# Performance work log

Measured on AMD Instinct MI355X. Metric: run time of the kernel, lower is better.

## Reference

```python
import jax, jax.numpy as jnp
import numpy as np

D = 1024       # latent_size
LW = 16        # leaf_width
DEPTH = 8      # tree depth
NN = 2**DEPTH - 1   # internal decision nodes
NL = 2**DEPTH       # leaves
B, S = 2, 1024


def _fff(x, nw, nb, w1, b1, w2, b2, act):
    """Hard-routed Fast FeedForward (eval mode).
    x: (B,S,D); nw: (NN,D); nb: (NN,); w1: (NL,D,LW); b1: (NL,LW);
    w2: (NL,LW,D); b2: (NL,D).
    """
    node = jnp.zeros(x.shape[:2], dtype=jnp.int32)
    for _ in range(DEPTH):
        logit = jnp.einsum('bsd,bsd->bs', x, nw[node]) + nb[node]
        node = 2 * node + 1 + (logit > 0).astype(jnp.int32)
    leaf = node - NN  # (B,S) in [0, NL)
    h = act(jnp.einsum('bsd,bsdl->bsl', x, w1[leaf]) + b1[leaf])
    return jnp.einsum('bsl,bsld->bsd', h, w2[leaf]) + b2[leaf]


def _forward(x,
             q_nw, q_nb, q_w1, q_b1, q_w2, q_b2,
             k_nw, k_nb, k_w1, k_b1, k_w2, k_b2,
             v_nw, v_nb, v_w1, v_b1, v_w2, v_b2,
             f_nw, f_nb, f_w1, f_b1, f_w2, f_b2):
    # manual norm (torch std is unbiased; note original divides by sqrt(std+eps))
    mu = jnp.mean(x, -1, keepdims=True)
    sd = jnp.std(x, -1, ddof=1, keepdims=True)
    xn = (x - mu) / jnp.sqrt(sd + 1e-5)
    relu = jax.nn.relu
    q = _fff(xn, q_nw, q_nb, q_w1, q_b1, q_w2, q_b2, relu)
    k = _fff(xn, k_nw, k_nb, k_w1, k_b1, k_w2, k_b2, relu)
    v = _fff(xn, v_nw, v_nb, v_w1, v_b1, v_w2, v_b2, relu)
    att = jax.nn.softmax(jnp.einsum('bqd,bkd->bqk', q, k) / jnp.sqrt(jnp.float32(D)), axis=-1)
    y = xn + jnp.einsum('bqk,bkd->bqd', att, v)
    gelu = lambda t: jax.nn.gelu(t, approximate=False)
    return y + _fff(y, f_nw, f_nb, f_w1, f_b1, f_w2, f_b2, gelu)


def _make_fff_params(key, scale_in, scale_leaf):
    ks = jax.random.split(key, 4)
    nw = jax.random.normal(ks[0], (NN, D), jnp.float32) * scale_in
    nb = jnp.zeros((NN,), jnp.float32)
    w1 = jax.random.normal(ks[1], (NL, D, LW), jnp.float32) * scale_in
    b1 = jax.random.normal(ks[2], (NL, LW), jnp.float32) * 0.01
    w2 = jax.random.normal(ks[3], (NL, LW, D), jnp.float32) * scale_leaf
    b2 = jnp.zeros((NL, D), jnp.float32)
    return nw, nb, w1, b1, w2, b2


def setup_inputs() -> dict:
    key = jax.random.key(0)
    kx, kq, kk, kv, kf = jax.random.split(key, 5)
    s_in = 1.0 / np.sqrt(D)
    s_lf = 1.0 / np.sqrt(LW)
    inp = {"x": jax.random.normal(kx, (B, S, D), jnp.float32)}
    for name, kk_ in (("q", kq), ("k", kk), ("v", kv), ("f", kf)):
        nw, nb, w1, b1, w2, b2 = _make_fff_params(kk_, s_in, s_lf)
        inp.update({f"{name}_nw": nw, f"{name}_nb": nb, f"{name}_w1": w1,
                    f"{name}_b1": b1, f"{name}_w2": w2, f"{name}_b2": b2})
    return inp


def reference(x,
              q_nw, q_nb, q_w1, q_b1, q_w2, q_b2,
              k_nw, k_nb, k_w1, k_b1, k_w2, k_b2,
              v_nw, v_nb, v_w1, v_b1, v_w2, v_b2,
              f_nw, f_nb, f_w1, f_b1, f_w2, f_b2):
    return _forward(x,
                    q_nw, q_nb, q_w1, q_b1, q_w2, q_b2,
                    k_nw, k_nb, k_w1, k_b1, k_w2, k_b2,
                    v_nw, v_nb, v_w1, v_b1, v_w2, v_b2,
                    f_nw, f_nb, f_w1, f_b1, f_w2, f_b2)
```

## Files before the change

kernel.cpp:

```cpp
#include <hip/hip_runtime.h>
#include <hip/hip_bf16.h>
#include <math.h>

#define DD 1024
#define LWW 16
#define NNODES 255
#define NLEAF 256
#define BB 2
#define SS 1024
#define NTOK (BB*SS)
#define PLANE ((size_t)NTOK * DD)
#define MS ((size_t)1024 * 1024)
#define MAXCHUNK 512
#define CH 8

typedef short bf16x8 __attribute__((ext_vector_type(8)));
typedef float f32x4 __attribute__((ext_vector_type(4)));

#define GLOBAL_AS __attribute__((address_space(1)))
#define LDS_AS __attribute__((address_space(3)))

__device__ __forceinline__ void gld_lds16(const void* g, void* l) {
  __builtin_amdgcn_global_load_lds((const GLOBAL_AS unsigned int*)g,
                                   (LDS_AS unsigned int*)l, 16, 0, 0);
}

__device__ __forceinline__ unsigned short f2bf(float f) {
  union { float f; unsigned int u; } v; v.f = f;
  unsigned int u = v.u;
  unsigned int lsb = (u >> 16) & 1u;
  u += 0x7fffu + lsb;
  return (unsigned short)(u >> 16);
}
__device__ __forceinline__ float bf2f(unsigned short h) {
  union { unsigned int u; float f; } v; v.u = ((unsigned int)h) << 16;
  return v.f;
}
__device__ __forceinline__ void split3(float a, unsigned short& h0,
                                       unsigned short& h1, unsigned short& h2) {
  h0 = f2bf(a);
  float r = a - bf2f(h0);
  h1 = f2bf(r);
  float r2 = r - bf2f(h1);
  h2 = f2bf(r2);
}

__global__ __launch_bounds__(256) void norm_kernel(const float* __restrict__ x,
                                                   float* __restrict__ xn) {
  int tok = blockIdx.x, tid = threadIdx.x;
  const float4 v = ((const float4*)(x + (size_t)tok * DD))[tid];
  double s = (double)v.x + (double)v.y + (double)v.z + (double)v.w;
  double s2 = (double)v.x * v.x + (double)v.y * v.y + (double)v.z * v.z + (double)v.w * v.w;
  for (int o = 32; o; o >>= 1) { s += __shfl_down(s, o); s2 += __shfl_down(s2, o); }
  __shared__ double rs[4], rs2[4];
  __shared__ float stats[2];
  int wid = tid >> 6, lane = tid & 63;
  if (lane == 0) { rs[wid] = s; rs2[wid] = s2; }
  __syncthreads();
  if (tid == 0) {
    double ts = rs[0] + rs[1] + rs[2] + rs[3];
    double ts2 = rs2[0] + rs2[1] + rs2[2] + rs2[3];
    double mu = ts / DD;
    double var = (ts2 - DD * mu * mu) / (DD - 1);
    if (var < 0) var = 0;
    double sd = sqrt(var);
    stats[0] = (float)mu;
    stats[1] = (float)(1.0 / sqrt(sd + 1e-5));
  }
  __syncthreads();
  float mu = stats[0], inv = stats[1];
  float4 o;
  o.x = (v.x - mu) * inv; o.y = (v.y - mu) * inv;
  o.z = (v.z - mu) * inv; o.w = (v.w - mu) * inv;
  ((float4*)(xn + (size_t)tok * DD))[tid] = o;
}

__global__ __launch_bounds__(256) void route_kernel(
    const float* __restrict__ xin,
    const float* nw0, const float* nb0,
    const float* nw1, const float* nb1,
    const float* nw2, const float* nb2,
    int* __restrict__ leaf_arr, int* __restrict__ hist, int ntree) {
  int tid = threadIdx.x, lane = tid & 63, wid = tid >> 6;
  int gw = blockIdx.x * 4 + wid;
  int tok = gw / ntree, tr = gw - tok * ntree;
  if (tok >= NTOK) return;
  const float* nws[3] = {nw0, nw1, nw2};
  const float* nbs[3] = {nb0, nb1, nb2};
  const float* nw = nws[tr];
  const float* nb = nbs[tr];
  f32x4 xq[4];
  const f32x4* xb = (const f32x4*)(xin + (size_t)tok * DD);
#pragma unroll
  for (int j = 0; j < 4; ++j) xq[j] = xb[lane + 64 * j];
  int node = 0;
#pragma unroll 1
  for (int step = 0; step < 8; ++step) {
    const f32x4* wb = (const f32x4*)(nw + (size_t)node * DD);
    double p = 0.0;
#pragma unroll
    for (int j = 0; j < 4; ++j) {
      f32x4 w = wb[lane + 64 * j];
      p += (double)xq[j][0] * w[0] + (double)xq[j][1] * w[1] +
           (double)xq[j][2] * w[2] + (double)xq[j][3] * w[3];
    }
#pragma unroll
    for (int o = 1; o < 64; o <<= 1) p += __shfl_xor(p, o);
    double logit = p + (double)nb[node];
    node = 2 * node + 1 + (logit > 0.0 ? 1 : 0);
  }
  if (lane == 0) {
    int leaf = node - NNODES;
    leaf_arr[(size_t)tr * NTOK + tok] = leaf;
    atomicAdd(&hist[tr * NLEAF + leaf], 1);
  }
}

__global__ __launch_bounds__(256) void scan_kernel(const int* __restrict__ hist,
                                                   int* __restrict__ offs,
                                                   int* __restrict__ cursor,
                                                   int4* __restrict__ desc,
                                                   int ntree, int tree0) {
  __shared__ int buf[256];
  __shared__ int dcnt;
  int tid = threadIdx.x;
  for (int tr = 0; tr < ntree; ++tr) {
    int slot = tree0 + tr;
    int v = hist[slot * NLEAF + tid];
    buf[tid] = v;
    if (tid == 0) dcnt = 0;
    __syncthreads();
    int run = v;
    for (int off = 1; off < 256; off <<= 1) {
      int add = (tid >= off) ? buf[tid - off] : 0;
      __syncthreads();
      run += add;
      buf[tid] = run;
      __syncthreads();
    }
    if (tid == 0) offs[slot * (NLEAF + 1)] = 0;
    offs[slot * (NLEAF + 1) + tid + 1] = run;
    cursor[slot * NLEAF + tid] = run - v;
    if (v > 0) {
      int k = (v + CH - 1) / CH;
      int base = atomicAdd(&dcnt, k);
      int lo = run - v;
      for (int j = 0; j < k; ++j) {
        int s = lo + j * CH;
        int e = min(run, s + CH);
        desc[slot * MAXCHUNK + base + j] = make_int4(tid, s, e, 0);
      }
    }
    __syncthreads();
  }
}

__global__ __launch_bounds__(256) void scatter_kernel(const int* __restrict__ leaf_arr,
                                                      int* __restrict__ cursor,
                                                      int* __restrict__ list,
                                                      int tree0, int ntree) {
  int tok = blockIdx.x * 256 + threadIdx.x;
  for (int tr = 0; tr < ntree; ++tr) {
    int slot = tree0 + tr;
    int leaf = leaf_arr[(size_t)slot * NTOK + tok];
    int pos = atomicAdd(&cursor[slot * NLEAF + leaf], 1);
    list[(size_t)slot * NTOK + pos] = tok;
  }
}

struct LeafW {
  const float* w1[3]; const float* b1[3]; const float* w2[3]; const float* b2[3];
  unsigned short* outs[3];
  float* out_res;
};

__global__ __launch_bounds__(256) void leafmlp_kernel(
    const float* __restrict__ xin,
    const int* __restrict__ list, const int4* __restrict__ desc,
    LeafW W, int tree0, int act) {
  int ty = blockIdx.y;
  int slot = tree0 + ty;
  int4 dsc = desc[slot * MAXCHUNK + blockIdx.x];
  int leaf = dsc.x;
  if (leaf < 0) return;
  int lo = dsc.y, hi = dsc.z;
  const int* L = list + (size_t)slot * NTOK;
  const float* W1 = W.w1[ty] + (size_t)leaf * DD * LWW;
  const float* B1 = W.b1[ty] + (size_t)leaf * LWW;
  const float* W2 = W.w2[ty] + (size_t)leaf * LWW * DD;
  const float* B2 = W.b2[ty] + (size_t)leaf * DD;
  unsigned short* osp = W.outs[ty];
  int tid = threadIdx.x;
  int lane = tid & 63, wid = tid >> 6;

  __shared__ float xsl[CH][1024];
  __shared__ float hpart[4][CH][20];
  __shared__ float hs[CH][16];

  float b1c = B1[tid & 15];

  int r = tid >> 2;
  const float* W1p = W1 + (size_t)r * 16 + (tid & 3) * 4;
  f32x4 wreg[16];
#pragma unroll
  for (int p = 0; p < 16; ++p) wreg[p] = *(const f32x4*)(W1p + (size_t)p * 1024);

  int toks[CH];
#pragma unroll
  for (int t = 0; t < CH; ++t) {
    int idx = lo + t;
    toks[t] = (idx < hi) ? L[idx] : -1;
    if (toks[t] >= 0) {
      float4 v = ((const float4*)(xin + (size_t)toks[t] * DD))[tid];
      *(float4*)&xsl[t][tid * 4] = v;
    } else {
      float4 z = {0.f, 0.f, 0.f, 0.f};
      *(float4*)&xsl[t][tid * 4] = z;
    }
  }
  __syncthreads();

  f32x4 part4[CH];
#pragma unroll
  for (int t = 0; t < CH; ++t) part4[t] = (f32x4){0.f, 0.f, 0.f, 0.f};
#pragma unroll
  for (int p = 0; p < 16; ++p) {
#pragma unroll
    for (int t = 0; t < CH; ++t) {
      float xv = xsl[t][p * 64 + r];
      part4[t] += xv * wreg[p];
    }
  }

  const float* W2p = W2 + tid * 4;
  f32x4 w2a[8];
#pragma unroll
  for (int l = 0; l < 8; ++l) w2a[l] = *(const f32x4*)(W2p + (size_t)l * 1024);
  f32x4 b2v = *(const f32x4*)(B2 + tid * 4);

#pragma unroll
  for (int t = 0; t < CH; ++t) {
    f32x4 v = part4[t];
#pragma unroll
    for (int o = 4; o < 64; o <<= 1) {
      v[0] += __shfl_xor(v[0], o);
      v[1] += __shfl_xor(v[1], o);
      v[2] += __shfl_xor(v[2], o);
      v[3] += __shfl_xor(v[3], o);
    }
    if (lane < 4) *(f32x4*)&hpart[wid][t][lane * 4] = v;
  }
  __syncthreads();

  if (tid < 16 * CH) {
    int t = tid >> 4, c = tid & 15;
    float h = b1c + hpart[0][t][c] + hpart[1][t][c] + hpart[2][t][c] + hpart[3][t][c];
    if (act == 0) h = fmaxf(h, 0.f);
    else h = 0.5f * h * (1.f + erff(h * 0.70710678118654752f));
    hs[t][c] = h;
  }
  __syncthreads();

  f32x4 w2b[8];
#pragma unroll
  for (int l = 0; l < 8; ++l) w2b[l] = *(const f32x4*)(W2p + (size_t)(8 + l) * 1024);
  f32x4 acc[CH];
#pragma unroll
  for (int t = 0; t < CH; ++t) acc[t] = b2v;
#pragma unroll
  for (int l = 0; l < 8; ++l) {
#pragma unroll
    for (int t = 0; t < CH; ++t) acc[t] += w2a[l] * hs[t][l];
  }
#pragma unroll
  for (int l = 0; l < 8; ++l) {
#pragma unroll
    for (int t = 0; t < CH; ++t) acc[t] += w2b[l] * hs[t][8 + l];
  }

#pragma unroll
  for (int t = 0; t < CH; ++t) {
    if (toks[t] < 0) break;
    size_t off = (size_t)toks[t] * DD + tid * 4;
    if (osp) {
      ushort4 o0, o1, o2;
      split3(acc[t][0], o0.x, o1.x, o2.x);
      split3(acc[t][1], o0.y, o1.y, o2.y);
      split3(acc[t][2], o0.z, o1.z, o2.z);
      split3(acc[t][3], o0.w, o1.w, o2.w);
      *(ushort4*)(osp + off) = o0;
      *(ushort4*)(osp + PLANE + off) = o1;
      *(ushort4*)(osp + 2 * PLANE + off) = o2;
    } else {
      float4 xr = *(const float4*)&xsl[t][tid * 4];
      float4 o;
      o.x = xr.x + acc[t][0];
      o.y = xr.y + acc[t][1];
      o.z = xr.z + acc[t][2];
      o.w = xr.w + acc[t][3];
      *(float4*)(W.out_res + off) = o;
    }
  }
}

__global__ __launch_bounds__(256) void transpose_v(const unsigned short* __restrict__ v,
                                                   unsigned short* __restrict__ vt) {
  __shared__ unsigned short t[32][34];
  int b = blockIdx.z & 1, p = blockIdx.z >> 1;
  int s0 = blockIdx.x * 32, d0 = blockIdx.y * 32;
  int tx = threadIdx.x, ty = threadIdx.y;
  const unsigned short* vb = v + p * PLANE + (size_t)b * SS * DD;
  unsigned short* vtb = vt + p * PLANE + (size_t)b * DD * SS;
#pragma unroll
  for (int k = 0; k < 4; ++k) {
    int r = ty + 8 * k;
    t[r][tx] = vb[(size_t)(s0 + r) * DD + d0 + tx];
  }
  __syncthreads();
#pragma unroll
  for (int k = 0; k < 4; ++k) {
    int r = ty + 8 * k;
    vtb[(size_t)(d0 + r) * SS + s0 + tx] = t[tx][r];
  }
}

#define BKK 64
__global__ __launch_bounds__(256) void gemm_nt3(
    const unsigned short* __restrict__ A,
    const unsigned short* __restrict__ Bt,
    float* __restrict__ C,
    const float* __restrict__ addsrc,
    float scale) {
  __shared__ short As[3][64 * BKK];
  __shared__ short Bs[3][64 * BKK];
  int b = blockIdx.z;
  int m0 = blockIdx.x * 64, n0 = blockIdx.y * 64;
  int tid = threadIdx.x, lane = tid & 63, wid = tid >> 6;
  int wm = wid >> 1, wn = wid & 1;
  f32x4 acc[2][2] = {};

  int sk0 = (((lane & 7) ^ (lane >> 3)) * 8);
  int srow0 = wid * 8 + (lane >> 3);
  int fr = lane & 15;
  int r7 = fr & 7;

  const unsigned short* Ap[3];
  const unsigned short* Bp[3];
#pragma unroll
  for (int p = 0; p < 3; ++p) {
    Ap[p] = A + p * PLANE + b * MS;
    Bp[p] = Bt + p * PLANE + b * MS;
  }

  for (int kt = 0; kt < 1024 / BKK; ++kt) {
    int kbase = kt * BKK;
#pragma unroll
    for (int p = 0; p < 3; ++p) {
#pragma unroll
      for (int r = 0; r < 2; ++r) {
        int row = r * 32 + srow0;
        gld_lds16(Ap[p] + (size_t)(m0 + row) * 1024 + kbase + sk0, &As[p][(r * 32 + wid * 8) * BKK]);
        gld_lds16(Bp[p] + (size_t)(n0 + row) * 1024 + kbase + sk0, &Bs[p][(r * 32 + wid * 8) * BKK]);
      }
    }
    __syncthreads();
#pragma unroll
    for (int kk = 0; kk < 2; ++kk) {
      int fkc = (((kk * 4 + (lane >> 4)) ^ r7) * 8);
      bf16x8 af[3][2], bfr[3][2];
#pragma unroll
      for (int p = 0; p < 3; ++p) {
        af[p][0]  = *(const bf16x8*)&As[p][(wm * 32 + fr) * BKK + fkc];
        af[p][1]  = *(const bf16x8*)&As[p][(wm * 32 + 16 + fr) * BKK + fkc];
        bfr[p][0] = *(const bf16x8*)&Bs[p][(wn * 32 + fr) * BKK + fkc];
        bfr[p][1] = *(const bf16x8*)&Bs[p][(wn * 32 + 16 + fr) * BKK + fkc];
      }
#pragma unroll
      for (int mi = 0; mi < 2; ++mi)
#pragma unroll
        for (int ni = 0; ni < 2; ++ni) {
          acc[mi][ni] = __builtin_amdgcn_mfma_f32_16x16x32_bf16(af[2][mi], bfr[0][ni], acc[mi][ni], 0, 0, 0);
          acc[mi][ni] = __builtin_amdgcn_mfma_f32_16x16x32_bf16(af[1][mi], bfr[1][ni], acc[mi][ni], 0, 0, 0);
          acc[mi][ni] = __builtin_amdgcn_mfma_f32_16x16x32_bf16(af[0][mi], bfr[2][ni], acc[mi][ni], 0, 0, 0);
          acc[mi][ni] = __builtin_amdgcn_mfma_f32_16x16x32_bf16(af[1][mi], bfr[0][ni], acc[mi][ni], 0, 0, 0);
          acc[mi][ni] = __builtin_amdgcn_mfma_f32_16x16x32_bf16(af[0][mi], bfr[1][ni], acc[mi][ni], 0, 0, 0);
          acc[mi][ni] = __builtin_amdgcn_mfma_f32_16x16x32_bf16(af[0][mi], bfr[0][ni], acc[mi][ni], 0, 0, 0);
        }
    }
    __syncthreads();
  }

  float* Cb = C + b * MS;
  const float* Rb = addsrc ? addsrc + b * MS : nullptr;
  int crow0 = (lane >> 4) * 4, ccol = lane & 15;
#pragma unroll
  for (int mi = 0; mi < 2; ++mi)
#pragma unroll
    for (int ni = 0; ni < 2; ++ni) {
      int colg = n0 + wn * 32 + ni * 16 + ccol;
#pragma unroll
      for (int j = 0; j < 4; ++j) {
        int rowg = m0 + wm * 32 + mi * 16 + crow0 + j;
        float vv = acc[mi][ni][j] * scale;
        if (Rb) vv += Rb[(size_t)rowg * 1024 + colg];
        Cb[(size_t)rowg * 1024 + colg] = vv;
      }
    }
}

__global__ __launch_bounds__(256) void softmax_kernel(const float* __restrict__ sc,
                                                      unsigned short* __restrict__ P) {
  int row = blockIdx.x, tid = threadIdx.x;
  int wid = tid >> 6, lane = tid & 63;
  const float4 v = ((const float4*)(sc + (size_t)row * SS))[tid];
  float mx = fmaxf(fmaxf(v.x, v.y), fmaxf(v.z, v.w));
  for (int o = 32; o; o >>= 1) mx = fmaxf(mx, __shfl_down(mx, o));
  __shared__ float red[4];
  __shared__ float bres[2];
  if (lane == 0) red[wid] = mx;
  __syncthreads();
  if (tid == 0) bres[0] = fmaxf(fmaxf(red[0], red[1]), fmaxf(red[2], red[3]));
  __syncthreads();
  float m = bres[0];
  float e0 = expf(v.x - m), e1 = expf(v.y - m), e2 = expf(v.z - m), e3 = expf(v.w - m);
  float s = e0 + e1 + e2 + e3;
  for (int o = 32; o; o >>= 1) s += __shfl_down(s, o);
  if (lane == 0) red[wid] = s;
  __syncthreads();
  if (tid == 0) bres[1] = red[0] + red[1] + red[2] + red[3];
  __syncthreads();
  float inv = 1.f / bres[1];
  float p0 = e0 * inv, p1 = e1 * inv, p2 = e2 * inv, p3 = e3 * inv;
  ushort4 o0, o1, o2;
  split3(p0, o0.x, o1.x, o2.x);
  split3(p1, o0.y, o1.y, o2.y);
  split3(p2, o0.z, o1.z, o2.z);
  split3(p3, o0.w, o1.w, o2.w);
  size_t off = (size_t)row * SS + tid * 4;
  *(ushort4*)(P + off) = o0;
  *(ushort4*)(P + PLANE + off) = o1;
  *(ushort4*)(P + 2 * PLANE + off) = o2;
}

extern "C" void kernel_launch(void* const* d_in, const int* in_sizes, int n_in,
                              void* d_out, int out_size, void* d_ws, size_t ws_size,
                              hipStream_t stream) {
  const float* x = (const float*)d_in[0];
  const float* qp[6]; const float* kp[6]; const float* vp[6]; const float* fp[6];
  for (int i = 0; i < 6; ++i) {
    qp[i] = (const float*)d_in[1 + i];
    kp[i] = (const float*)d_in[7 + i];
    vp[i] = (const float*)d_in[13 + i];
    fp[i] = (const float*)d_in[19 + i];
  }
  char* ws = (char*)d_ws;
  float* xn           = (float*)(ws);
  unsigned short* qb  = (unsigned short*)(ws + ( 8 << 20));
  unsigned short* kb  = (unsigned short*)(ws + (20 << 20));
  unsigned short* vs  = (unsigned short*)(ws + (32 << 20));
  unsigned short* vt  = (unsigned short*)(ws + (44 << 20));
  float* sc           = (float*)(ws + (32 << 20));
  unsigned short* P   = (unsigned short*)(ws + ( 8 << 20));
  float* y            = (float*)(ws + (20 << 20));
  int* meta           = (int*)(ws + (56 << 20));
  int* hist           = meta;
  int* cursor         = meta + 1024;
  int* offs           = meta + 2048;
  int* leaf_arr       = meta + 4096;
  int* list           = meta + 12288;
  int4* desc          = (int4*)(meta + 20480);
  float* out          = (float*)d_out;

  hipMemsetAsync(hist, 0, 1024 * sizeof(int), stream);
  hipMemsetAsync(desc, 0xFF, 4 * MAXCHUNK * sizeof(int4), stream);
  norm_kernel<<<NTOK, 256, 0, stream>>>(x, xn);
  route_kernel<<<NTOK * 3 / 4, 256, 0, stream>>>(xn, qp[0], qp[1], kp[0], kp[1], vp[0], vp[1],
                                                 leaf_arr, hist, 3);
  scan_kernel<<<1, 256, 0, stream>>>(hist, offs, cursor, desc, 3, 0);
  scatter_kernel<<<NTOK / 256, 256, 0, stream>>>(leaf_arr, cursor, list, 0, 3);

  LeafW Wqkv;
  Wqkv.w1[0] = qp[2]; Wqkv.b1[0] = qp[3]; Wqkv.w2[0] = qp[4]; Wqkv.b2[0] = qp[5];
  Wqkv.w1[1] = kp[2]; Wqkv.b1[1] = kp[3]; Wqkv.w2[1] = kp[4]; Wqkv.b2[1] = kp[5];
  Wqkv.w1[2] = vp[2]; Wqkv.b1[2] = vp[3]; Wqkv.w2[2] = vp[4]; Wqkv.b2[2] = vp[5];
  Wqkv.outs[0] = qb; Wqkv.outs[1] = kb; Wqkv.outs[2] = vs;
  Wqkv.out_res = nullptr;
  leafmlp_kernel<<<dim3(MAXCHUNK, 3), 256, 0, stream>>>(xn, list, desc, Wqkv, 0, 0);

  transpose_v<<<dim3(32, 32, 6), dim3(32, 8), 0, stream>>>(vs, vt);
  gemm_nt3<<<dim3(16, 16, 2), 256, 0, stream>>>(qb, kb, sc, nullptr, 0.03125f);
  softmax_kernel<<<NTOK, 256, 0, stream>>>(sc, P);
  gemm_nt3<<<dim3(16, 16, 2), 256, 0, stream>>>(P, vt, y, xn, 1.0f);

  route_kernel<<<NTOK / 4, 256, 0, stream>>>(y, fp[0], fp[1], fp[0], fp[1], fp[0], fp[1],
                                             leaf_arr + 3 * NTOK, hist + 3 * NLEAF, 1);
  scan_kernel<<<1, 256, 0, stream>>>(hist, offs, cursor, desc, 1, 3);
  scatter_kernel<<<NTOK / 256, 256, 0, stream>>>(leaf_arr, cursor, list, 3, 1);

  LeafW Wf;
  Wf.w1[0] = fp[2]; Wf.b1[0] = fp[3]; Wf.w2[0] = fp[4]; Wf.b2[0] = fp[5];
  Wf.w1[1] = fp[2]; Wf.b1[1] = fp[3]; Wf.w2[1] = fp[4]; Wf.b2[1] = fp[5];
  Wf.w1[2] = fp[2]; Wf.b1[2] = fp[3]; Wf.w2[2] = fp[4]; Wf.b2[2] = fp[5];
  Wf.outs[0] = nullptr; Wf.outs[1] = nullptr; Wf.outs[2] = nullptr;
  Wf.out_res = out;
  leafmlp_kernel<<<dim3(MAXCHUNK, 1), 256, 0, stream>>>(y, list, desc, Wf, 3, 1);
}
```

Baseline: 188.6 us.

## Fuse norm with routing, scan with scatter, and split-K the QK GEMM

Layer norm and the three q/k/v tree routings now run in one kernel, with the normalized row staged in LDS. Histogram scan, descriptor fill (replacing a memset) and token scatter are merged into one single-block kernel using LDS cursors. The QK^T score GEMM is split along K into two halves that atomically add into a zeroed buffer, doubling the grid. This removes several launches and intermediate round trips, at the cost of a serial single-block scatter over all tokens, float atomics, an extra memset, and order-dependent rounding in the scores.

```diff
diff --git a/kernel.cpp b/kernel.cpp
--- a/kernel.cpp
+++ b/kernel.cpp
@@ -45,16 +45,21 @@
   h2 = f2bf(r2);
 }
 
-__global__ __launch_bounds__(256) void norm_kernel(const float* __restrict__ x,
-                                                   float* __restrict__ xn) {
+__global__ __launch_bounds__(256) void norm_route_kernel(
+    const float* __restrict__ x, float* __restrict__ xn,
+    const float* nw0, const float* nb0,
+    const float* nw1, const float* nb1,
+    const float* nw2, const float* nb2,
+    int* __restrict__ leaf_arr, int* __restrict__ hist) {
   int tok = blockIdx.x, tid = threadIdx.x;
+  int wid = tid >> 6, lane = tid & 63;
+  __shared__ double rs[4], rs2[4];
+  __shared__ float stats[2];
+  __shared__ float xs[1024];
   const float4 v = ((const float4*)(x + (size_t)tok * DD))[tid];
   double s = (double)v.x + (double)v.y + (double)v.z + (double)v.w;
   double s2 = (double)v.x * v.x + (double)v.y * v.y + (double)v.z * v.z + (double)v.w * v.w;
   for (int o = 32; o; o >>= 1) { s += __shfl_down(s, o); s2 += __shfl_down(s2, o); }
-  __shared__ double rs[4], rs2[4];
-  __shared__ float stats[2];
-  int wid = tid >> 6, lane = tid & 63;
   if (lane == 0) { rs[wid] = s; rs2[wid] = s2; }
   __syncthreads();
   if (tid == 0) {
@@ -73,6 +78,39 @@
   o.x = (v.x - mu) * inv; o.y = (v.y - mu) * inv;
   o.z = (v.z - mu) * inv; o.w = (v.w - mu) * inv;
   ((float4*)(xn + (size_t)tok * DD))[tid] = o;
+  *(float4*)&xs[tid * 4] = o;
+  __syncthreads();
+
+  if (wid < 3) {
+    const float* nws[3] = {nw0, nw1, nw2};
+    const float* nbs[3] = {nb0, nb1, nb2};
+    const float* nw = nws[wid];
+    const float* nb = nbs[wid];
+    f32x4 xq[4];
+#pragma unroll
+    for (int j = 0; j < 4; ++j) xq[j] = *(const f32x4*)&xs[(lane + 64 * j) * 4];
+    int node = 0;
+#pragma unroll 1
+    for (int step = 0; step < 8; ++step) {
+      const f32x4* wb = (const f32x4*)(nw + (size_t)node * DD);
+      double p = 0.0;
+#pragma unroll
+      for (int j = 0; j < 4; ++j) {
+        f32x4 w = wb[lane + 64 * j];
+        p += (double)xq[j][0] * w[0] + (double)xq[j][1] * w[1] +
+             (double)xq[j][2] * w[2] + (double)xq[j][3] * w[3];
+      }
+#pragma unroll
+      for (int o2 = 1; o2 < 64; o2 <<= 1) p += __shfl_xor(p, o2);
+      double logit = p + (double)nb[node];
+      node = 2 * node + 1 + (logit > 0.0 ? 1 : 0);
+    }
+    if (lane == 0) {
+      int leaf = node - NNODES;
+      leaf_arr[(size_t)wid * NTOK + tok] = leaf;
+      atomicAdd(&hist[wid * NLEAF + leaf], 1);
+    }
+  }
 }
 
 __global__ __launch_bounds__(256) void route_kernel(
@@ -116,12 +154,12 @@
   }
 }
 
-__global__ __launch_bounds__(256) void scan_kernel(const int* __restrict__ hist,
-                                                   int* __restrict__ offs,
-                                                   int* __restrict__ cursor,
-                                                   int4* __restrict__ desc,
-                                                   int ntree, int tree0) {
+__global__ __launch_bounds__(256) void scan_scatter_kernel(
+    const int* __restrict__ hist, const int* __restrict__ leaf_arr,
+    int* __restrict__ list, int4* __restrict__ desc,
+    int ntree, int tree0) {
   __shared__ int buf[256];
+  __shared__ int cur[256];
   __shared__ int dcnt;
   int tid = threadIdx.x;
   for (int tr = 0; tr < ntree; ++tr) {
@@ -138,9 +176,7 @@
       buf[tid] = run;
       __syncthreads();
     }
-    if (tid == 0) offs[slot * (NLEAF + 1)] = 0;
-    offs[slot * (NLEAF + 1) + tid + 1] = run;
-    cursor[slot * NLEAF + tid] = run - v;
+    cur[tid] = run - v;
     if (v > 0) {
       int k = (v + CH - 1) / CH;
       int base = atomicAdd(&dcnt, k);
@@ -152,19 +188,15 @@
       }
     }
     __syncthreads();
-  }
-}
-
-__global__ __launch_bounds__(256) void scatter_kernel(const int* __restrict__ leaf_arr,
-                                                      int* __restrict__ cursor,
-                                                      int* __restrict__ list,
-                                                      int tree0, int ntree) {
-  int tok = blockIdx.x * 256 + threadIdx.x;
-  for (int tr = 0; tr < ntree; ++tr) {
-    int slot = tree0 + tr;
-    int leaf = leaf_arr[(size_t)slot * NTOK + tok];
-    int pos = atomicAdd(&cursor[slot * NLEAF + leaf], 1);
-    list[(size_t)slot * NTOK + pos] = tok;
+    for (int i = dcnt + tid; i < MAXCHUNK; i += 256)
+      desc[slot * MAXCHUNK + i] = make_int4(-1, 0, 0, 0);
+    for (int base = 0; base < NTOK; base += 256) {
+      int tok = base + tid;
+      int leaf = leaf_arr[(size_t)slot * NTOK + tok];
+      int pos = atomicAdd(&cur[leaf], 1);
+      list[(size_t)slot * NTOK + pos] = tok;
+    }
+    __syncthreads();
   }
 }
 
@@ -408,6 +440,87 @@
     }
 }
 
+__global__ __launch_bounds__(256) void gemm_nt3_ks(
+    const unsigned short* __restrict__ A,
+    const unsigned short* __restrict__ Bt,
+    float* __restrict__ C,
+    float scale) {
+  __shared__ short As[3][64 * BKK];
+  __shared__ short Bs[3][64 * BKK];
+  int b = blockIdx.z & 1, kh = blockIdx.z >> 1;
+  int m0 = blockIdx.x * 64, n0 = blockIdx.y * 64;
+  int tid = threadIdx.x, lane = tid & 63, wid = tid >> 6;
+  int wm = wid >> 1, wn = wid & 1;
+  f32x4 acc[2][2] = {};
+
+  int sk0 = (((lane & 7) ^ (lane >> 3)) * 8);
+  int srow0 = wid * 8 + (lane >> 3);
+  int fr = lane & 15;
+  int r7 = fr & 7;
+
+  const unsigned short* Ap[3];
+  const unsigned short* Bp[3];
+#pragma unroll
+  for (int p = 0; p < 3; ++p) {
+    Ap[p] = A + p * PLANE + b * MS;
+    Bp[p] = Bt + p * PLANE + b * MS;
+  }
+
+  for (int kt = kh * 8; kt < kh * 8 + 8; ++kt) {
+    int kbase = kt * BKK;
+#pragma unroll
+    for (int p = 0; p < 3; ++p) {
+#pragma unroll
+      for (int r = 0; r < 2; ++r) {
+        int row = r * 32 + srow0;
+        gld_lds16(Ap[p] + (size_t)(m0 + row) * 1024 + kbase + sk0, &As[p][(r * 32 + wid * 8) * BKK]);
+        gld_lds16(Bp[p] + (size_t)(n0 + row) * 1024 + kbase + sk0, &Bs[p][(r * 32 + wid * 8) * BKK]);
+      }
+    }
+    __syncthreads();
+#pragma unroll
+    for (int kk = 0; kk < 2; ++kk) {
+      int fkc = (((kk * 4 + (lane >> 4)) ^ r7) * 8);
+      bf16x8 af[3][2], bfr[3][2];
+#pragma unroll
+      for (int p = 0; p < 3; ++p) {
+        af[p][0]  = *(const bf16x8*)&As[p][(wm * 32 + fr) * BKK + fkc];
+        af[p][1]  = *(const bf16x8*)&As[p][(wm * 32 + 16 + fr) * BKK + fkc];
+        bfr[p][0] = *(const bf16x8*)&Bs[p][(wn * 32 + fr) * BKK + fkc];
+        bfr[p][1] = *(const bf16x8*)&Bs[p][(wn * 32 + 16 + fr) * BKK + fkc];
+      }
+#pragma unroll
+      for (int mi = 0; mi < 2; ++mi)
+#pragma unroll
+        for (int ni = 0; ni < 2; ++ni) {
+          acc[mi][ni] = __builtin_amdgcn_mfma_f32_16x16x32_bf16(af[2][mi], bfr[0][ni], acc[mi][ni], 0, 0, 0);
+          acc[mi][ni] = __builtin_amdgcn_mfma_f32_16x16x32_bf16(af[1][mi], bfr[1][ni], acc[mi][ni], 0, 0, 0);
+          acc[mi][ni] = __builtin_amdgcn_mfma_f32_16x16x32_bf16(af[0][mi], bfr[2][ni], acc[mi][ni], 0, 0, 0);
+          acc[mi][ni] = __builtin_amdgcn_mfma_f32_16x16x32_bf16(af[1][mi], bfr[0][ni], acc[mi][ni], 0, 0, 0);
+          acc[mi][ni] = __builtin_amdgcn_mfma_f32_16x16x32_bf16(af[0][mi], bfr[1][ni], acc[mi][ni], 0, 0, 0);
+          acc[mi][ni] = __builtin_amdgcn_mfma_f32_16x16x32_bf16(af[0][mi], bfr[0][ni], acc[mi][ni], 0, 0, 0);
+        }
+    }
+    __syncthreads();
+  }
+
+  float* Cb = C + b * MS;
+  int crow0 = (lane >> 4) * 4, ccol = lane & 15;
+#pragma unroll
+  for (int mi = 0; mi < 2; ++mi)
+#pragma unroll
+    for (int ni = 0; ni < 2; ++ni) {
+      int colg = n0 + wn * 32 + ni * 16 + ccol;
+#pragma unroll
+      for (int j = 0; j < 4; ++j) {
+        int rowg = m0 + wm * 32 + mi * 16 + crow0 + j;
+        float vv = acc[mi][ni][j] * scale;
+        __hip_atomic_fetch_add(&Cb[(size_t)rowg * 1024 + colg], vv,
+                               __ATOMIC_RELAXED, __HIP_MEMORY_SCOPE_AGENT);
+      }
+    }
+}
+
 __global__ __launch_bounds__(256) void softmax_kernel(const float* __restrict__ sc,
                                                       unsigned short* __restrict__ P) {
   int row = blockIdx.x, tid = threadIdx.x;
@@ -464,20 +577,15 @@
   float* y            = (float*)(ws + (20 << 20));
   int* meta           = (int*)(ws + (56 << 20));
   int* hist           = meta;
-  int* cursor         = meta + 1024;
-  int* offs           = meta + 2048;
   int* leaf_arr       = meta + 4096;
   int* list           = meta + 12288;
   int4* desc          = (int4*)(meta + 20480);
   float* out          = (float*)d_out;
 
   hipMemsetAsync(hist, 0, 1024 * sizeof(int), stream);
-  hipMemsetAsync(desc, 0xFF, 4 * MAXCHUNK * sizeof(int4), stream);
-  norm_kernel<<<NTOK, 256, 0, stream>>>(x, xn);
-  route_kernel<<<NTOK * 3 / 4, 256, 0, stream>>>(xn, qp[0], qp[1], kp[0], kp[1], vp[0], vp[1],
-                                                 leaf_arr, hist, 3);
-  scan_kernel<<<1, 256, 0, stream>>>(hist, offs, cursor, desc, 3, 0);
-  scatter_kernel<<<NTOK / 256, 256, 0, stream>>>(leaf_arr, cursor, list, 0, 3);
+  norm_route_kernel<<<NTOK, 256, 0, stream>>>(x, xn, qp[0], qp[1], kp[0], kp[1], vp[0], vp[1],
+                                              leaf_arr, hist);
+  scan_scatter_kernel<<<1, 256, 0, stream>>>(hist, leaf_arr, list, desc, 3, 0);
 
   LeafW Wqkv;
   Wqkv.w1[0] = qp[2]; Wqkv.b1[0] = qp[3]; Wqkv.w2[0] = qp[4]; Wqkv.b2[0] = qp[5];
@@ -488,14 +596,14 @@
   leafmlp_kernel<<<dim3(MAXCHUNK, 3), 256, 0, stream>>>(xn, list, desc, Wqkv, 0, 0);
 
   transpose_v<<<dim3(32, 32, 6), dim3(32, 8), 0, stream>>>(vs, vt);
-  gemm_nt3<<<dim3(16, 16, 2), 256, 0, stream>>>(qb, kb, sc, nullptr, 0.03125f);
+  hipMemsetAsync(sc, 0, (size_t)2 * 1024 * 1024 * sizeof(float), stream);
+  gemm_nt3_ks<<<dim3(16, 16, 4), 256, 0, stream>>>(qb, kb, sc, 0.03125f);
   softmax_kernel<<<NTOK, 256, 0, stream>>>(sc, P);
   gemm_nt3<<<dim3(16, 16, 2), 256, 0, stream>>>(P, vt, y, xn, 1.0f);
 
   route_kernel<<<NTOK / 4, 256, 0, stream>>>(y, fp[0], fp[1], fp[0], fp[1], fp[0], fp[1],
                                              leaf_arr + 3 * NTOK, hist + 3 * NLEAF, 1);
-  scan_kernel<<<1, 256, 0, stream>>>(hist, offs, cursor, desc, 1, 3);
-  scatter_kernel<<<NTOK / 256, 256, 0, stream>>>(leaf_arr, cursor, list, 3, 1);
+  scan_scatter_kernel<<<1, 256, 0, stream>>>(hist, leaf_arr, list, desc, 1, 3);
 
   LeafW Wf;
   Wf.w1[0] = fp[2]; Wf.b1[0] = fp[3]; Wf.w2[0] = fp[4]; Wf.b2[0] = fp[5];
```

Result: slower. 194.5 us (+3.1%).
